# Kernel optimization log

Measured on AMD Instinct MI355X. Metric: run time of the kernel, lower is better.

Reference implementation:

```python
import jax, jax.numpy as jnp
import numpy as np

TOP_K = 8
N_GROUP = 8
TOPK_GROUP = 4
ROUTED_SCALING_FACTOR = 2.5
NORM_TOPK_PROB = True
TOKENS = 16384
HIDDEN = 4096
N_EXPERTS = 256


def setup_inputs() -> dict:
    key = jax.random.key(0)
    k1, k2, k3 = jax.random.split(key, 3)
    x = jax.random.normal(k1, (TOKENS, HIDDEN), dtype=jnp.float32)
    weight = jax.random.normal(k2, (N_EXPERTS, HIDDEN), dtype=jnp.float32) * 0.02
    e_score_correction_bias = jax.random.normal(k3, (N_EXPERTS,), dtype=jnp.float32) * 0.01
    return {"x": x, "weight": weight, "e_score_correction_bias": e_score_correction_bias}


def reference(x, weight, e_score_correction_bias):
    # gates: [T, E]
    gates = x @ weight.T
    orig_scores = jax.nn.sigmoid(gates.astype(jnp.float32))
    scores = orig_scores + e_score_correction_bias
    T, E = scores.shape
    eg = E // N_GROUP  # experts per group
    s = scores.reshape(T, N_GROUP, eg)
    # group score = sum of top-2 expert scores within each group -> [T, G]
    group_scores = jax.lax.top_k(s, 2)[0].sum(axis=-1)
    # torch code selects the (n_group - topk_group) SMALLEST groups and keeps
    # only those (masked_fill zeroes everything else) -- replicate faithfully.
    k_drop = N_GROUP - TOPK_GROUP
    _, bottom_idx = jax.lax.top_k(-group_scores, k_drop)  # [T, k_drop]
    keep = jnp.zeros((T, N_GROUP), dtype=bool).at[jnp.arange(T)[:, None], bottom_idx].set(True)
    s = jnp.where(keep[:, :, None], s, 0.0).reshape(T, E)
    # torch.topk(-scores) -> indices of the k SMALLEST scores
    _, inds = jax.lax.top_k(-s, TOP_K)  # [T, top_k]
    sel = jnp.take_along_axis(orig_scores, inds, axis=-1)
    if TOP_K > 1 and NORM_TOPK_PROB:
        sel = sel / (sel.sum(axis=-1, keepdims=True) + 1e-20)
    sel = sel * ROUTED_SCALING_FACTOR
    return inds, sel
```

## Files before the change

kernel.cpp:

```cpp
#include <hip/hip_runtime.h>
#include <hip/hip_fp16.h>
#include <cstdint>
#include <cmath>

#define TOKENS  16384
#define HIDDEN  4096
#define NEXP    256
#define TOPK    8
#define KDROP   4

typedef _Float16 f16x8  __attribute__((ext_vector_type(8)));
typedef float    f32x16 __attribute__((ext_vector_type(16)));
typedef float    f32x4  __attribute__((ext_vector_type(4)));

#define LO_SCALE 2048.0f
#define LO_INV   (1.0f/2048.0f)

#define WS_G0_OFF 0
#define WS_G1_OFF 16777216
#define WS_WH_OFF 33554432
#define WS_WL_OFF 35651584

static __device__ __forceinline__ f32x4 ldnt4(const float* p) {
    return __builtin_nontemporal_load((const f32x4*)p);
}
static __device__ __forceinline__ void stnt(float* p, float v) {
    __builtin_nontemporal_store(v, p);
}

__global__ __launch_bounds__(256)
void wsplit(const float* __restrict__ w, _Float16* __restrict__ wh,
            _Float16* __restrict__ wl)
{
    const int idx = blockIdx.x * 256 + threadIdx.x;
    const int e   = idx >> 9;
    const int kg8 = idx & 511;
    const float* p = w + (size_t)e * HIDDEN + kg8 * 8;
    f32x4 f0 = ldnt4(p);
    f32x4 f1 = ldnt4(p + 4);
    float v[8] = {f0.x, f0.y, f0.z, f0.w, f1.x, f1.y, f1.z, f1.w};
    f16x8 hi, lo;
    #pragma unroll
    for (int i = 0; i < 8; ++i) {
        _Float16 h = (_Float16)v[i];
        hi[i] = h;
        lo[i] = (_Float16)((v[i] - (float)h) * LO_SCALE);
    }
    const int kc = kg8 >> 2, s = (kg8 >> 1) & 1, hl = kg8 & 1;
    const int cid = ((kc * 2 + s) * 8 + (e >> 5)) * 64 + hl * 32 + (e & 31);
    ((f16x8*)wh)[cid] = hi;
    ((f16x8*)wl)[cid] = lo;
}

__global__ __launch_bounds__(256, 2)
void gemm_split(const float* __restrict__ x, const _Float16* __restrict__ wh,
                const _Float16* __restrict__ wl,
                float* __restrict__ g0, float* __restrict__ g1)
{
    __shared__ _Float16 Ah[2][64 * 32];
    __shared__ _Float16 Al[2][64 * 32];

    const int tid  = threadIdx.x;
    const int wv   = tid >> 6;
    const int lane = tid & 63;

    const int bid    = blockIdx.x;
    const int y      = (bid >> 2) & 1;
    const int tokblk = (bid >> 3) * 4 + (bid & 3);
    const int tok0   = tokblk * 64;
    const int kcg0   = y * 64;
    float* gates_half = y ? g1 : g0;

    const int sm = tid >> 2;
    const int sq = tid & 3;
    const float* xr = x + (size_t)(tok0 + sm) * HIDDEN;
    const int scid = ((sq >> 1) * 2 + (sm >> 5)) * 64 + (sq & 1) * 32 + (sm & 31);

    const f16x8* whc = (const f16x8*)wh;
    const f16x8* wlc = (const f16x8*)wl;

    f32x16 accH[2][2] = {};
    f32x16 accX[2][2] = {};

    f16x8 bh[2][2], bl[2][2];

    {
        const float* ap = xr + kcg0 * 32 + sq * 8;
        f32x4 f0 = ldnt4(ap);
        f32x4 f1 = ldnt4(ap + 4);
        #pragma unroll
        for (int s = 0; s < 2; ++s) {
            const int base = ((kcg0 * 2 + s) * 8 + wv * 2) * 64 + lane;
            bh[s][0] = whc[base];
            bh[s][1] = whc[base + 64];
            bl[s][0] = wlc[base];
            bl[s][1] = wlc[base + 64];
        }
        float v[8] = {f0.x, f0.y, f0.z, f0.w, f1.x, f1.y, f1.z, f1.w};
        f16x8 hi, lo;
        #pragma unroll
        for (int i = 0; i < 8; ++i) {
            _Float16 h = (_Float16)v[i];
            hi[i] = h;
            lo[i] = (_Float16)((v[i] - (float)h) * LO_SCALE);
        }
        *(f16x8*)&Ah[0][scid * 8] = hi;
        *(f16x8*)&Al[0][scid * 8] = lo;
    }
    __syncthreads();

    #pragma unroll 2
    for (int kc = 0; kc < 64; ++kc) {
        const int cur  = kc & 1;
        const bool more = (kc < 63);

        f32x4 a0n, a1n;
        f16x8 bhn[2][2], bln[2][2];
        if (more) {
            const int kcg = kcg0 + kc + 1;
            const float* ap = xr + kcg * 32 + sq * 8;
            a0n = ldnt4(ap);
            a1n = ldnt4(ap + 4);
            #pragma unroll
            for (int s = 0; s < 2; ++s) {
                const int base = ((kcg * 2 + s) * 8 + wv * 2) * 64 + lane;
                bhn[s][0] = whc[base];
                bhn[s][1] = whc[base + 64];
                bln[s][0] = wlc[base];
                bln[s][1] = wlc[base + 64];
            }
        }

        #pragma unroll
        for (int s = 0; s < 2; ++s) {
            f16x8 ah0 = *(const f16x8*)&Ah[cur][((s * 2 + 0) * 64 + lane) * 8];
            f16x8 ah1 = *(const f16x8*)&Ah[cur][((s * 2 + 1) * 64 + lane) * 8];
            f16x8 al0 = *(const f16x8*)&Al[cur][((s * 2 + 0) * 64 + lane) * 8];
            f16x8 al1 = *(const f16x8*)&Al[cur][((s * 2 + 1) * 64 + lane) * 8];

            accH[0][0] = __builtin_amdgcn_mfma_f32_32x32x16_f16(ah0, bh[s][0], accH[0][0], 0, 0, 0);
            accH[0][1] = __builtin_amdgcn_mfma_f32_32x32x16_f16(ah0, bh[s][1], accH[0][1], 0, 0, 0);
            accH[1][0] = __builtin_amdgcn_mfma_f32_32x32x16_f16(ah1, bh[s][0], accH[1][0], 0, 0, 0);
            accH[1][1] = __builtin_amdgcn_mfma_f32_32x32x16_f16(ah1, bh[s][1], accH[1][1], 0, 0, 0);
            accX[0][0] = __builtin_amdgcn_mfma_f32_32x32x16_f16(al0, bh[s][0], accX[0][0], 0, 0, 0);
            accX[0][1] = __builtin_amdgcn_mfma_f32_32x32x16_f16(al0, bh[s][1], accX[0][1], 0, 0, 0);
            accX[1][0] = __builtin_amdgcn_mfma_f32_32x32x16_f16(al1, bh[s][0], accX[1][0], 0, 0, 0);
            accX[1][1] = __builtin_amdgcn_mfma_f32_32x32x16_f16(al1, bh[s][1], accX[1][1], 0, 0, 0);
            accX[0][0] = __builtin_amdgcn_mfma_f32_32x32x16_f16(ah0, bl[s][0], accX[0][0], 0, 0, 0);
            accX[0][1] = __builtin_amdgcn_mfma_f32_32x32x16_f16(ah0, bl[s][1], accX[0][1], 0, 0, 0);
            accX[1][0] = __builtin_amdgcn_mfma_f32_32x32x16_f16(ah1, bl[s][0], accX[1][0], 0, 0, 0);
            accX[1][1] = __builtin_amdgcn_mfma_f32_32x32x16_f16(ah1, bl[s][1], accX[1][1], 0, 0, 0);
        }

        if (more) {
            float v[8] = {a0n.x, a0n.y, a0n.z, a0n.w, a1n.x, a1n.y, a1n.z, a1n.w};
            f16x8 hi, lo;
            #pragma unroll
            for (int i = 0; i < 8; ++i) {
                _Float16 h = (_Float16)v[i];
                hi[i] = h;
                lo[i] = (_Float16)((v[i] - (float)h) * LO_SCALE);
            }
            *(f16x8*)&Ah[cur ^ 1][scid * 8] = hi;
            *(f16x8*)&Al[cur ^ 1][scid * 8] = lo;
            #pragma unroll
            for (int s = 0; s < 2; ++s) {
                bh[s][0] = bhn[s][0]; bh[s][1] = bhn[s][1];
                bl[s][0] = bln[s][0]; bl[s][1] = bln[s][1];
            }
        }
        __syncthreads();
    }

    const int col   = lane & 31;
    const int rbase = 4 * (lane >> 5);
    #pragma unroll
    for (int r = 0; r < 2; ++r)
        #pragma unroll
        for (int c = 0; c < 2; ++c) {
            float* gp = gates_half + (size_t)(tok0 + r * 32) * NEXP + wv * 64 + c * 32 + col;
            #pragma unroll
            for (int reg = 0; reg < 16; ++reg) {
                const int row = (reg & 3) + 8 * (reg >> 2) + rbase;
                stnt(gp + (size_t)row * NEXP, accH[r][c][reg] + accX[r][c][reg] * LO_INV);
            }
        }
}

__device__ __forceinline__ unsigned ordkey(float f) {
    unsigned u = __float_as_uint(f);
    return (u & 0x80000000u) ? ~u : (u | 0x80000000u);
}

__global__ __launch_bounds__(256, 4)
void gate_epilogue(const float* __restrict__ g0,
                   const float* __restrict__ g1,
                   const float* __restrict__ bias,
                   float* __restrict__ out)
{
    const int tid  = threadIdx.x;
    const int wv   = tid >> 6;
    const int lane = tid & 63;
    const int t    = blockIdx.x * 4 + wv;

    f32x4 ga = ldnt4(g0 + (size_t)t * NEXP + lane * 4);
    f32x4 gb = ldnt4(g1 + (size_t)t * NEXP + lane * 4);
    float4 bv = ((const float4*)bias)[lane];
    float4 gv = make_float4(ga.x + gb.x, ga.y + gb.y, ga.z + gb.z, ga.w + gb.w);

    float sig0 = 1.0f / (1.0f + expf(-gv.x));
    float sig1 = 1.0f / (1.0f + expf(-gv.y));
    float sig2 = 1.0f / (1.0f + expf(-gv.z));
    float sig3 = 1.0f / (1.0f + expf(-gv.w));
    float sc0 = sig0 + bv.x, sc1 = sig1 + bv.y;
    float sc2 = sig2 + bv.z, sc3 = sig3 + bv.w;

    float m1 = fmaxf(sc0, sc1);
    float m2 = fminf(sc0, sc1);
    if (sc2 > m1) { m2 = m1; m1 = sc2; } else m2 = fmaxf(m2, sc2);
    if (sc3 > m1) { m2 = m1; m1 = sc3; } else m2 = fmaxf(m2, sc3);
    #pragma unroll
    for (int off = 1; off < 8; off <<= 1) {
        float o1 = __shfl_xor(m1, off);
        float o2 = __shfl_xor(m2, off);
        float nm1 = fmaxf(m1, o1);
        float nm2 = fmaxf(fminf(m1, o1), fmaxf(m2, o2));
        m1 = nm1; m2 = nm2;
    }
    float gsum = m1 + m2;
    float gs[8];
    #pragma unroll
    for (int gi = 0; gi < 8; ++gi) gs[gi] = __shfl(gsum, gi * 8);

    int keepmask = 0;
    #pragma unroll
    for (int g = 0; g < 8; ++g) {
        int rank = 0;
        #pragma unroll
        for (int h = 0; h < 8; ++h)
            rank += (gs[h] < gs[g]) || (gs[h] == gs[g] && h < g);
        if (rank < KDROP) keepmask |= (1 << g);
    }
    const bool kept = (keepmask >> (lane >> 3)) & 1;

    const unsigned ib = (unsigned)(lane * 4);
    unsigned long long k0 = ((unsigned long long)ordkey(kept ? sc0 : 0.0f) << 32) | (ib + 0);
    unsigned long long k1 = ((unsigned long long)ordkey(kept ? sc1 : 0.0f) << 32) | (ib + 1);
    unsigned long long k2 = ((unsigned long long)ordkey(kept ? sc2 : 0.0f) << 32) | (ib + 2);
    unsigned long long k3 = ((unsigned long long)ordkey(kept ? sc3 : 0.0f) << 32) | (ib + 3);

    float ssum = 0.0f, myval = 0.0f;
    int myidx = 0;
    #pragma unroll
    for (int r = 0; r < TOPK; ++r) {
        unsigned long long kmin = k0 < k1 ? k0 : k1;
        if (k2 < kmin) kmin = k2;
        if (k3 < kmin) kmin = k3;
        #pragma unroll
        for (int off = 32; off >= 1; off >>= 1) {
            unsigned long long o = __shfl_xor(kmin, off);
            if (o < kmin) kmin = o;
        }
        const int id   = (int)(kmin & 0xffffffffull);
        const int src  = id >> 2;
        const int slot = id & 3;
        float vsrc = (slot == 0) ? sig0 : (slot == 1) ? sig1
                   : (slot == 2) ? sig2 : sig3;
        float v = __shfl(vsrc, src);
        ssum += v;
        if (lane == r) { myidx = id; myval = v; }
        const bool mine = (lane == src);
        if (mine && slot == 0) k0 = ~0ull;
        if (mine && slot == 1) k1 = ~0ull;
        if (mine && slot == 2) k2 = ~0ull;
        if (mine && slot == 3) k3 = ~0ull;
    }

    if (lane < TOPK) {
        out[(size_t)t * TOPK + lane] = (float)myidx;
        out[(size_t)TOKENS * TOPK + (size_t)t * TOPK + lane] =
            myval / (ssum + 1e-20f) * 2.5f;
    }
}

extern "C" void kernel_launch(void* const* d_in, const int* in_sizes, int n_in,
                              void* d_out, int out_size, void* d_ws, size_t ws_size,
                              hipStream_t stream)
{
    const float* x    = (const float*)d_in[0];
    const float* w    = (const float*)d_in[1];
    const float* bias = (const float*)d_in[2];
    float* out = (float*)d_out;

    float*     g0 = (float*)((char*)d_ws + WS_G0_OFF);
    float*     g1 = (float*)((char*)d_ws + WS_G1_OFF);
    _Float16*  wh = (_Float16*)((char*)d_ws + WS_WH_OFF);
    _Float16*  wl = (_Float16*)((char*)d_ws + WS_WL_OFF);

    wsplit<<<dim3(512), dim3(256), 0, stream>>>(w, wh, wl);
    gemm_split<<<dim3(512), dim3(256), 0, stream>>>(x, wh, wl, g0, g1);
    gate_epilogue<<<dim3(TOKENS / 4), dim3(256), 0, stream>>>(g0, g1, bias, out);
}
```

Baseline: 440.1 us.

## Fuse gate GEMM with sigmoid/top-k epilogue, dropping split-K gate buffers

Merges the GEMM and the routing epilogue into one kernel. Each block now handles 32 tokens over the full K dimension instead of 64 tokens over half of K. Sigmoid scores go into a 32 KB shared buffer, and each wave then runs group selection and top-k for 8 tokens. This removes the two 16 MB fp32 partial-gate writes, their re-read and one kernel launch. In exchange, the M tile is halved, so each block issues twice as many weight loads per MFMA. The larger shared memory footprint may also reduce occupancy, and the serial per-token epilogue sits at the end of every block.

After: 489.7 us. +11.3%, slower.

```diff
diff --git a/kernel.cpp b/kernel.cpp
--- a/kernel.cpp
+++ b/kernel.cpp
@@ -10,22 +10,18 @@
 #define KDROP   4
 
 typedef _Float16 f16x8  __attribute__((ext_vector_type(8)));
+typedef _Float16 f16x4  __attribute__((ext_vector_type(4)));
 typedef float    f32x16 __attribute__((ext_vector_type(16)));
 typedef float    f32x4  __attribute__((ext_vector_type(4)));
 
 #define LO_SCALE 2048.0f
 #define LO_INV   (1.0f/2048.0f)
 
-#define WS_G0_OFF 0
-#define WS_G1_OFF 16777216
-#define WS_WH_OFF 33554432
-#define WS_WL_OFF 35651584
+#define WS_WH_OFF 0
+#define WS_WL_OFF 2097152
 
 static __device__ __forceinline__ f32x4 ldnt4(const float* p) {
     return __builtin_nontemporal_load((const f32x4*)p);
-}
-static __device__ __forceinline__ void stnt(float* p, float v) {
-    __builtin_nontemporal_store(v, p);
 }
 
 __global__ __launch_bounds__(256)
@@ -52,78 +48,72 @@
     ((f16x8*)wl)[cid] = lo;
 }
 
+__device__ __forceinline__ unsigned ordkey(float f) {
+    unsigned u = __float_as_uint(f);
+    return (u & 0x80000000u) ? ~u : (u | 0x80000000u);
+}
+
 __global__ __launch_bounds__(256, 2)
-void gemm_split(const float* __restrict__ x, const _Float16* __restrict__ wh,
-                const _Float16* __restrict__ wl,
-                float* __restrict__ g0, float* __restrict__ g1)
+void gemm_gate(const float* __restrict__ x, const _Float16* __restrict__ wh,
+               const _Float16* __restrict__ wl,
+               const float* __restrict__ bias, float* __restrict__ out)
 {
-    __shared__ _Float16 Ah[2][64 * 32];
-    __shared__ _Float16 Al[2][64 * 32];
+    __shared__ _Float16 Ah[2][32 * 32];
+    __shared__ _Float16 Al[2][32 * 32];
+    __shared__ float sigbuf[32 * 256];
 
     const int tid  = threadIdx.x;
     const int wv   = tid >> 6;
     const int lane = tid & 63;
-
-    const int bid    = blockIdx.x;
-    const int y      = (bid >> 2) & 1;
-    const int tokblk = (bid >> 3) * 4 + (bid & 3);
-    const int tok0   = tokblk * 64;
-    const int kcg0   = y * 64;
-    float* gates_half = y ? g1 : g0;
-
-    const int sm = tid >> 2;
-    const int sq = tid & 3;
-    const float* xr = x + (size_t)(tok0 + sm) * HIDDEN;
-    const int scid = ((sq >> 1) * 2 + (sm >> 5)) * 64 + (sq & 1) * 32 + (sm & 31);
+    const int tok0 = blockIdx.x * 32;
+
+    const int sm = tid >> 3;
+    const int sq = tid & 7;
+    const float* xr = x + (size_t)(tok0 + sm) * HIDDEN + sq * 4;
+    const int sidx = ((sq >> 2) * 64 + ((sq >> 1) & 1) * 32 + sm) * 8 + (sq & 1) * 4;
 
     const f16x8* whc = (const f16x8*)wh;
     const f16x8* wlc = (const f16x8*)wl;
 
-    f32x16 accH[2][2] = {};
-    f32x16 accX[2][2] = {};
+    f32x16 accH[2] = {};
+    f32x16 accX[2] = {};
 
     f16x8 bh[2][2], bl[2][2];
 
     {
-        const float* ap = xr + kcg0 * 32 + sq * 8;
-        f32x4 f0 = ldnt4(ap);
-        f32x4 f1 = ldnt4(ap + 4);
+        f32x4 a = ldnt4(xr);
         #pragma unroll
         for (int s = 0; s < 2; ++s) {
-            const int base = ((kcg0 * 2 + s) * 8 + wv * 2) * 64 + lane;
+            const int base = (s * 8 + wv * 2) * 64 + lane;
             bh[s][0] = whc[base];
             bh[s][1] = whc[base + 64];
             bl[s][0] = wlc[base];
             bl[s][1] = wlc[base + 64];
         }
-        float v[8] = {f0.x, f0.y, f0.z, f0.w, f1.x, f1.y, f1.z, f1.w};
-        f16x8 hi, lo;
-        #pragma unroll
-        for (int i = 0; i < 8; ++i) {
-            _Float16 h = (_Float16)v[i];
+        f16x4 hi, lo;
+        #pragma unroll
+        for (int i = 0; i < 4; ++i) {
+            _Float16 h = (_Float16)a[i];
             hi[i] = h;
-            lo[i] = (_Float16)((v[i] - (float)h) * LO_SCALE);
-        }
-        *(f16x8*)&Ah[0][scid * 8] = hi;
-        *(f16x8*)&Al[0][scid * 8] = lo;
+            lo[i] = (_Float16)((a[i] - (float)h) * LO_SCALE);
+        }
+        *(f16x4*)&Ah[0][sidx] = hi;
+        *(f16x4*)&Al[0][sidx] = lo;
     }
     __syncthreads();
 
     #pragma unroll 2
-    for (int kc = 0; kc < 64; ++kc) {
+    for (int kc = 0; kc < 128; ++kc) {
         const int cur  = kc & 1;
-        const bool more = (kc < 63);
-
-        f32x4 a0n, a1n;
+        const bool more = (kc < 127);
+
+        f32x4 an;
         f16x8 bhn[2][2], bln[2][2];
         if (more) {
-            const int kcg = kcg0 + kc + 1;
-            const float* ap = xr + kcg * 32 + sq * 8;
-            a0n = ldnt4(ap);
-            a1n = ldnt4(ap + 4);
+            an = ldnt4(xr + (kc + 1) * 32);
             #pragma unroll
             for (int s = 0; s < 2; ++s) {
-                const int base = ((kcg * 2 + s) * 8 + wv * 2) * 64 + lane;
+                const int base = (((kc + 1) * 2 + s) * 8 + wv * 2) * 64 + lane;
                 bhn[s][0] = whc[base];
                 bhn[s][1] = whc[base + 64];
                 bln[s][0] = wlc[base];
@@ -133,36 +123,27 @@
 
         #pragma unroll
         for (int s = 0; s < 2; ++s) {
-            f16x8 ah0 = *(const f16x8*)&Ah[cur][((s * 2 + 0) * 64 + lane) * 8];
-            f16x8 ah1 = *(const f16x8*)&Ah[cur][((s * 2 + 1) * 64 + lane) * 8];
-            f16x8 al0 = *(const f16x8*)&Al[cur][((s * 2 + 0) * 64 + lane) * 8];
-            f16x8 al1 = *(const f16x8*)&Al[cur][((s * 2 + 1) * 64 + lane) * 8];
-
-            accH[0][0] = __builtin_amdgcn_mfma_f32_32x32x16_f16(ah0, bh[s][0], accH[0][0], 0, 0, 0);
-            accH[0][1] = __builtin_amdgcn_mfma_f32_32x32x16_f16(ah0, bh[s][1], accH[0][1], 0, 0, 0);
-            accH[1][0] = __builtin_amdgcn_mfma_f32_32x32x16_f16(ah1, bh[s][0], accH[1][0], 0, 0, 0);
-            accH[1][1] = __builtin_amdgcn_mfma_f32_32x32x16_f16(ah1, bh[s][1], accH[1][1], 0, 0, 0);
-            accX[0][0] = __builtin_amdgcn_mfma_f32_32x32x16_f16(al0, bh[s][0], accX[0][0], 0, 0, 0);
-            accX[0][1] = __builtin_amdgcn_mfma_f32_32x32x16_f16(al0, bh[s][1], accX[0][1], 0, 0, 0);
-            accX[1][0] = __builtin_amdgcn_mfma_f32_32x32x16_f16(al1, bh[s][0], accX[1][0], 0, 0, 0);
-            accX[1][1] = __builtin_amdgcn_mfma_f32_32x32x16_f16(al1, bh[s][1], accX[1][1], 0, 0, 0);
-            accX[0][0] = __builtin_amdgcn_mfma_f32_32x32x16_f16(ah0, bl[s][0], accX[0][0], 0, 0, 0);
-            accX[0][1] = __builtin_amdgcn_mfma_f32_32x32x16_f16(ah0, bl[s][1], accX[0][1], 0, 0, 0);
-            accX[1][0] = __builtin_amdgcn_mfma_f32_32x32x16_f16(ah1, bl[s][0], accX[1][0], 0, 0, 0);
-            accX[1][1] = __builtin_amdgcn_mfma_f32_32x32x16_f16(ah1, bl[s][1], accX[1][1], 0, 0, 0);
+            f16x8 ah = *(const f16x8*)&Ah[cur][(s * 64 + lane) * 8];
+            f16x8 al = *(const f16x8*)&Al[cur][(s * 64 + lane) * 8];
+
+            accH[0] = __builtin_amdgcn_mfma_f32_32x32x16_f16(ah, bh[s][0], accH[0], 0, 0, 0);
+            accH[1] = __builtin_amdgcn_mfma_f32_32x32x16_f16(ah, bh[s][1], accH[1], 0, 0, 0);
+            accX[0] = __builtin_amdgcn_mfma_f32_32x32x16_f16(al, bh[s][0], accX[0], 0, 0, 0);
+            accX[1] = __builtin_amdgcn_mfma_f32_32x32x16_f16(al, bh[s][1], accX[1], 0, 0, 0);
+            accX[0] = __builtin_amdgcn_mfma_f32_32x32x16_f16(ah, bl[s][0], accX[0], 0, 0, 0);
+            accX[1] = __builtin_amdgcn_mfma_f32_32x32x16_f16(ah, bl[s][1], accX[1], 0, 0, 0);
         }
 
         if (more) {
-            float v[8] = {a0n.x, a0n.y, a0n.z, a0n.w, a1n.x, a1n.y, a1n.z, a1n.w};
-            f16x8 hi, lo;
-            #pragma unroll
-            for (int i = 0; i < 8; ++i) {
-                _Float16 h = (_Float16)v[i];
+            f16x4 hi, lo;
+            #pragma unroll
+            for (int i = 0; i < 4; ++i) {
+                _Float16 h = (_Float16)an[i];
                 hi[i] = h;
-                lo[i] = (_Float16)((v[i] - (float)h) * LO_SCALE);
-            }
-            *(f16x8*)&Ah[cur ^ 1][scid * 8] = hi;
-            *(f16x8*)&Al[cur ^ 1][scid * 8] = lo;
+                lo[i] = (_Float16)((an[i] - (float)h) * LO_SCALE);
+            }
+            *(f16x4*)&Ah[cur ^ 1][sidx] = hi;
+            *(f16x4*)&Al[cur ^ 1][sidx] = lo;
             #pragma unroll
             for (int s = 0; s < 2; ++s) {
                 bh[s][0] = bhn[s][0]; bh[s][1] = bhn[s][1];
@@ -172,114 +153,96 @@
         __syncthreads();
     }
 
-    const int col   = lane & 31;
-    const int rbase = 4 * (lane >> 5);
-    #pragma unroll
-    for (int r = 0; r < 2; ++r)
+    {
+        const int col   = lane & 31;
+        const int rbase = 4 * (lane >> 5);
         #pragma unroll
         for (int c = 0; c < 2; ++c) {
-            float* gp = gates_half + (size_t)(tok0 + r * 32) * NEXP + wv * 64 + c * 32 + col;
             #pragma unroll
             for (int reg = 0; reg < 16; ++reg) {
                 const int row = (reg & 3) + 8 * (reg >> 2) + rbase;
-                stnt(gp + (size_t)row * NEXP, accH[r][c][reg] + accX[r][c][reg] * LO_INV);
-            }
-        }
-}
-
-__device__ __forceinline__ unsigned ordkey(float f) {
-    unsigned u = __float_as_uint(f);
-    return (u & 0x80000000u) ? ~u : (u | 0x80000000u);
-}
-
-__global__ __launch_bounds__(256, 4)
-void gate_epilogue(const float* __restrict__ g0,
-                   const float* __restrict__ g1,
-                   const float* __restrict__ bias,
-                   float* __restrict__ out)
-{
-    const int tid  = threadIdx.x;
-    const int wv   = tid >> 6;
-    const int lane = tid & 63;
-    const int t    = blockIdx.x * 4 + wv;
-
-    f32x4 ga = ldnt4(g0 + (size_t)t * NEXP + lane * 4);
-    f32x4 gb = ldnt4(g1 + (size_t)t * NEXP + lane * 4);
-    float4 bv = ((const float4*)bias)[lane];
-    float4 gv = make_float4(ga.x + gb.x, ga.y + gb.y, ga.z + gb.z, ga.w + gb.w);
-
-    float sig0 = 1.0f / (1.0f + expf(-gv.x));
-    float sig1 = 1.0f / (1.0f + expf(-gv.y));
-    float sig2 = 1.0f / (1.0f + expf(-gv.z));
-    float sig3 = 1.0f / (1.0f + expf(-gv.w));
-    float sc0 = sig0 + bv.x, sc1 = sig1 + bv.y;
-    float sc2 = sig2 + bv.z, sc3 = sig3 + bv.w;
-
-    float m1 = fmaxf(sc0, sc1);
-    float m2 = fminf(sc0, sc1);
-    if (sc2 > m1) { m2 = m1; m1 = sc2; } else m2 = fmaxf(m2, sc2);
-    if (sc3 > m1) { m2 = m1; m1 = sc3; } else m2 = fmaxf(m2, sc3);
-    #pragma unroll
-    for (int off = 1; off < 8; off <<= 1) {
-        float o1 = __shfl_xor(m1, off);
-        float o2 = __shfl_xor(m2, off);
-        float nm1 = fmaxf(m1, o1);
-        float nm2 = fmaxf(fminf(m1, o1), fmaxf(m2, o2));
-        m1 = nm1; m2 = nm2;
-    }
-    float gsum = m1 + m2;
-    float gs[8];
-    #pragma unroll
-    for (int gi = 0; gi < 8; ++gi) gs[gi] = __shfl(gsum, gi * 8);
-
-    int keepmask = 0;
-    #pragma unroll
-    for (int g = 0; g < 8; ++g) {
-        int rank = 0;
-        #pragma unroll
-        for (int h = 0; h < 8; ++h)
-            rank += (gs[h] < gs[g]) || (gs[h] == gs[g] && h < g);
-        if (rank < KDROP) keepmask |= (1 << g);
-    }
-    const bool kept = (keepmask >> (lane >> 3)) & 1;
-
-    const unsigned ib = (unsigned)(lane * 4);
-    unsigned long long k0 = ((unsigned long long)ordkey(kept ? sc0 : 0.0f) << 32) | (ib + 0);
-    unsigned long long k1 = ((unsigned long long)ordkey(kept ? sc1 : 0.0f) << 32) | (ib + 1);
-    unsigned long long k2 = ((unsigned long long)ordkey(kept ? sc2 : 0.0f) << 32) | (ib + 2);
-    unsigned long long k3 = ((unsigned long long)ordkey(kept ? sc3 : 0.0f) << 32) | (ib + 3);
-
-    float ssum = 0.0f, myval = 0.0f;
-    int myidx = 0;
-    #pragma unroll
-    for (int r = 0; r < TOPK; ++r) {
-        unsigned long long kmin = k0 < k1 ? k0 : k1;
-        if (k2 < kmin) kmin = k2;
-        if (k3 < kmin) kmin = k3;
-        #pragma unroll
-        for (int off = 32; off >= 1; off >>= 1) {
-            unsigned long long o = __shfl_xor(kmin, off);
-            if (o < kmin) kmin = o;
-        }
-        const int id   = (int)(kmin & 0xffffffffull);
-        const int src  = id >> 2;
-        const int slot = id & 3;
-        float vsrc = (slot == 0) ? sig0 : (slot == 1) ? sig1
-                   : (slot == 2) ? sig2 : sig3;
-        float v = __shfl(vsrc, src);
-        ssum += v;
-        if (lane == r) { myidx = id; myval = v; }
-        const bool mine = (lane == src);
-        if (mine && slot == 0) k0 = ~0ull;
-        if (mine && slot == 1) k1 = ~0ull;
-        if (mine && slot == 2) k2 = ~0ull;
-        if (mine && slot == 3) k3 = ~0ull;
-    }
-
-    if (lane < TOPK) {
-        out[(size_t)t * TOPK + lane] = (float)myidx;
-        out[(size_t)TOKENS * TOPK + (size_t)t * TOPK + lane] =
-            myval / (ssum + 1e-20f) * 2.5f;
+                const float g = accH[c][reg] + accX[c][reg] * LO_INV;
+                sigbuf[row * NEXP + wv * 64 + c * 32 + col] = 1.0f / (1.0f + expf(-g));
+            }
+        }
+    }
+    __syncthreads();
+
+    const float4 bv = ((const float4*)bias)[lane];
+    for (int tt = 0; tt < 8; ++tt) {
+        const int lt = wv * 8 + tt;
+        const int t  = tok0 + lt;
+        f32x4 sv = *(const f32x4*)&sigbuf[lt * NEXP + lane * 4];
+        const float sig0 = sv.x, sig1 = sv.y, sig2 = sv.z, sig3 = sv.w;
+        const float sc0 = sig0 + bv.x, sc1 = sig1 + bv.y;
+        const float sc2 = sig2 + bv.z, sc3 = sig3 + bv.w;
+
+        float m1 = fmaxf(sc0, sc1);
+        float m2 = fminf(sc0, sc1);
+        if (sc2 > m1) { m2 = m1; m1 = sc2; } else m2 = fmaxf(m2, sc2);
+        if (sc3 > m1) { m2 = m1; m1 = sc3; } else m2 = fmaxf(m2, sc3);
+        #pragma unroll
+        for (int off = 1; off < 8; off <<= 1) {
+            float o1 = __shfl_xor(m1, off);
+            float o2 = __shfl_xor(m2, off);
+            float nm1 = fmaxf(m1, o1);
+            float nm2 = fmaxf(fminf(m1, o1), fmaxf(m2, o2));
+            m1 = nm1; m2 = nm2;
+        }
+        float gsum = m1 + m2;
+        float gs[8];
+        #pragma unroll
+        for (int gi = 0; gi < 8; ++gi) gs[gi] = __shfl(gsum, gi * 8);
+
+        int keepmask = 0;
+        #pragma unroll
+        for (int g = 0; g < 8; ++g) {
+            int rank = 0;
+            #pragma unroll
+            for (int h = 0; h < 8; ++h)
+                rank += (gs[h] < gs[g]) || (gs[h] == gs[g] && h < g);
+            if (rank < KDROP) keepmask |= (1 << g);
+        }
+        const bool kept = (keepmask >> (lane >> 3)) & 1;
+
+        const unsigned ib = (unsigned)(lane * 4);
+        unsigned long long k0 = ((unsigned long long)ordkey(kept ? sc0 : 0.0f) << 32) | (ib + 0);
+        unsigned long long k1 = ((unsigned long long)ordkey(kept ? sc1 : 0.0f) << 32) | (ib + 1);
+        unsigned long long k2 = ((unsigned long long)ordkey(kept ? sc2 : 0.0f) << 32) | (ib + 2);
+        unsigned long long k3 = ((unsigned long long)ordkey(kept ? sc3 : 0.0f) << 32) | (ib + 3);
+
+        float ssum = 0.0f, myval = 0.0f;
+        int myidx = 0;
+        #pragma unroll
+        for (int r = 0; r < TOPK; ++r) {
+            unsigned long long kmin = k0 < k1 ? k0 : k1;
+            if (k2 < kmin) kmin = k2;
+            if (k3 < kmin) kmin = k3;
+            #pragma unroll
+            for (int off = 32; off >= 1; off >>= 1) {
+                unsigned long long o = __shfl_xor(kmin, off);
+                if (o < kmin) kmin = o;
+            }
+            const int id   = (int)(kmin & 0xffffffffull);
+            const int src  = id >> 2;
+            const int slot = id & 3;
+            float vsrc = (slot == 0) ? sig0 : (slot == 1) ? sig1
+                       : (slot == 2) ? sig2 : sig3;
+            float v = __shfl(vsrc, src);
+            ssum += v;
+            if (lane == r) { myidx = id; myval = v; }
+            const bool mine = (lane == src);
+            if (mine && slot == 0) k0 = ~0ull;
+            if (mine && slot == 1) k1 = ~0ull;
+            if (mine && slot == 2) k2 = ~0ull;
+            if (mine && slot == 3) k3 = ~0ull;
+        }
+
+        if (lane < TOPK) {
+            out[(size_t)t * TOPK + lane] = (float)myidx;
+            out[(size_t)TOKENS * TOPK + (size_t)t * TOPK + lane] =
+                myval / (ssum + 1e-20f) * 2.5f;
+        }
     }
 }
 
@@ -292,12 +255,9 @@
     const float* bias = (const float*)d_in[2];
     float* out = (float*)d_out;
 
-    float*     g0 = (float*)((char*)d_ws + WS_G0_OFF);
-    float*     g1 = (float*)((char*)d_ws + WS_G1_OFF);
     _Float16*  wh = (_Float16*)((char*)d_ws + WS_WH_OFF);
     _Float16*  wl = (_Float16*)((char*)d_ws + WS_WL_OFF);
 
     wsplit<<<dim3(512), dim3(256), 0, stream>>>(w, wh, wl);
-    gemm_split<<<dim3(512), dim3(256), 0, stream>>>(x, wh, wl, g0, g1);
-    gate_epilogue<<<dim3(TOKENS / 4), dim3(256), 0, stream>>>(g0, g1, bias, out);
-}
+    gemm_gate<<<dim3(TOKENS / 32), dim3(256), 0, stream>>>(x, wh, wl, bias, out);
+}
```
